# Kernel optimization log

Hardware: AMD Instinct MI355X
Metric: run time of the kernel (lower is better)

Reference implementation:

```python
import jax, jax.numpy as jnp
import numpy as np

NUM_CLASSES = 80
FOCAL_ALPHA = 0.25
FOCAL_GAMMA = 2.0
HUBER_SIGMA = 3.0
REG_MEAN = 0.0
REG_STD = 0.2
IMG_H = 800.0
IMG_W = 800.0
B, A, M = 4, 100000, 32


def setup_inputs() -> dict:
    key = jax.random.key(0)
    k1, k2, k3, k4, k5, k6, k7 = jax.random.split(key, 7)
    classification = jax.random.uniform(k1, (B, A, NUM_CLASSES), dtype=jnp.float32)
    regression = jax.random.normal(k2, (B, A, 4), dtype=jnp.float32)
    # plausible anchors: centers inside image, sizes 16..256
    cx = jax.random.uniform(k3, (A,), minval=0.0, maxval=IMG_W)
    cy = jax.random.uniform(k4, (A,), minval=0.0, maxval=IMG_H)
    s = jax.random.uniform(k5, (A, 2), minval=16.0, maxval=256.0)
    anchors = jnp.stack([cx - s[:, 0] / 2, cy - s[:, 1] / 2,
                         cx + s[:, 0] / 2, cy + s[:, 1] / 2], axis=1).astype(jnp.float32)
    # annotations: [B, M, 5] = x1,y1,x2,y2,class
    xy = jax.random.uniform(k6, (B, M, 2), minval=0.0, maxval=650.0)
    wh = jax.random.uniform(k7, (B, M, 2), minval=30.0, maxval=150.0)
    cls = jax.random.randint(jax.random.fold_in(key, 9), (B, M, 1), 0, NUM_CLASSES).astype(jnp.float32)
    annotations = jnp.concatenate([xy, xy + wh, cls], axis=-1)
    return {"classification": classification, "regression": regression,
            "anchors": anchors, "annotations": annotations}


def _pairwise_iou(anchors, boxes):
    # anchors [A,4], boxes [M,4] -> [A,M]
    ix1 = jnp.maximum(anchors[:, None, 0], boxes[None, :, 0])
    iy1 = jnp.maximum(anchors[:, None, 1], boxes[None, :, 1])
    ix2 = jnp.minimum(anchors[:, None, 2], boxes[None, :, 2])
    iy2 = jnp.minimum(anchors[:, None, 3], boxes[None, :, 3])
    inter = jnp.clip(ix2 - ix1, 0.0) * jnp.clip(iy2 - iy1, 0.0)
    area_a = (anchors[:, 2] - anchors[:, 0]) * (anchors[:, 3] - anchors[:, 1])
    area_b = (boxes[:, 2] - boxes[:, 0]) * (boxes[:, 3] - boxes[:, 1])
    union = area_a[:, None] + area_b[None, :] - inter
    return inter / jnp.maximum(union, 1e-8)


def _targets(anchors, annotations):
    # per-image anchor assignment, vmapped over batch
    def per_image(ann):
        boxes = ann[:, :4]
        cls = ann[:, 4].astype(jnp.int32)
        ious = _pairwise_iou(anchors, boxes)          # [A,M]
        best = jnp.argmax(ious, axis=1)               # [A]
        best_iou = jnp.max(ious, axis=1)
        pos = best_iou >= 0.5
        ign = (best_iou > 0.4) & (~pos)
        states = jnp.where(pos, 1.0, jnp.where(ign, -1.0, 0.0))
        cx = (anchors[:, 0] + anchors[:, 2]) * 0.5
        cy = (anchors[:, 1] + anchors[:, 3]) * 0.5
        inside = (cx >= 0) & (cx < IMG_W) & (cy >= 0) & (cy < IMG_H)
        states = jnp.where(inside, states, -1.0)
        labels = jax.nn.one_hot(cls[best], NUM_CLASSES, dtype=jnp.float32) * pos[:, None]
        ab = boxes[best]                              # assigned gt boxes [A,4]
        aw = anchors[:, 2] - anchors[:, 0]
        ah = anchors[:, 3] - anchors[:, 1]
        t = jnp.stack([(ab[:, 0] - anchors[:, 0]) / aw,
                       (ab[:, 1] - anchors[:, 1]) / ah,
                       (ab[:, 2] - anchors[:, 2]) / aw,
                       (ab[:, 3] - anchors[:, 3]) / ah], axis=1)
        t = (t - REG_MEAN) / REG_STD
        return labels, t, states
    return jax.vmap(per_image)(annotations)


def reference(classification, regression, anchors, annotations):
    labels, reg_t, states = _targets(anchors, annotations)   # [B,A,K],[B,A,4],[B,A]
    num_pos = jnp.maximum(jnp.sum((states == 1.0).astype(jnp.float32)), 1.0)
    # focal loss over non-ignored anchors
    valid = (states != -1.0)[..., None].astype(jnp.float32)
    p = jnp.clip(classification, 1e-4, 1.0 - 1e-4)
    bce = -(labels * jnp.log(p) + (1.0 - labels) * jnp.log1p(-p))
    alpha_f = jnp.where(labels == 1.0, FOCAL_ALPHA, 1.0 - FOCAL_ALPHA)
    focal_w = alpha_f * jnp.where(labels == 1.0, 1.0 - p, p) ** FOCAL_GAMMA
    cls_loss = jnp.sum(focal_w * bce * valid) / num_pos
    # smooth L1 over positive anchors
    pos_m = (states == 1.0)[..., None].astype(jnp.float32)
    s2 = HUBER_SIGMA ** 2
    d = jnp.abs(regression - reg_t)
    l1 = jnp.where(d < 1.0 / s2, 0.5 * s2 * d * d, d - 0.5 / s2)
    reg_loss = jnp.sum(l1 * pos_m) / num_pos
    return cls_loss + reg_loss
```

## Files before the change

### kernel.cpp

```cpp
#include <hip/hip_runtime.h>

#define BB 4
#define AA 100000
#define MM 32
#define NC 80
#define GX 391
#define NBLK (GX * BB)


__global__ __launch_bounds__(256) void fused_kernel(
    const float* __restrict__ anchors,
    const float* __restrict__ annotations,
    const float* __restrict__ regression,
    const float* __restrict__ cls,
    float* __restrict__ cls_part,
    float* __restrict__ reg_part,
    unsigned* __restrict__ pos_part)
{
    __shared__ float ann[MM * 5];
    __shared__ int scode[256];
    const int b = blockIdx.y;
    const int tid = threadIdx.x;
    if (tid < MM * 5) ann[tid] = annotations[b * MM * 5 + tid];
    __syncthreads();

    const int abase = blockIdx.x * 256;
    const int a = abase + tid;
    float reg_sum = 0.0f;
    int pos_cnt = 0;
    int code = -2;

    if (a < AA) {
        const float4 an = ((const float4*)anchors)[a];
        const float ax1 = an.x, ay1 = an.y, ax2 = an.z, ay2 = an.w;
        const float area_a = __fmul_rn(__fsub_rn(ax2, ax1), __fsub_rn(ay2, ay1));

        float best_iou = -1.0f;
        int best = 0;
        #pragma unroll
        for (int j = 0; j < MM; ++j) {
            const float bx1 = ann[j * 5 + 0];
            const float by1 = ann[j * 5 + 1];
            const float bx2 = ann[j * 5 + 2];
            const float by2 = ann[j * 5 + 3];
            const float ix1 = fmaxf(ax1, bx1);
            const float iy1 = fmaxf(ay1, by1);
            const float ix2 = fminf(ax2, bx2);
            const float iy2 = fminf(ay2, by2);
            const float iw = fmaxf(__fsub_rn(ix2, ix1), 0.0f);
            const float ih = fmaxf(__fsub_rn(iy2, iy1), 0.0f);
            const float inter = __fmul_rn(iw, ih);
            const float area_b = __fmul_rn(__fsub_rn(bx2, bx1), __fsub_rn(by2, by1));
            const float uni = __fsub_rn(__fadd_rn(area_a, area_b), inter);
            const float iou = __fdiv_rn(inter, fmaxf(uni, 1e-8f));
            if (iou > best_iou) { best_iou = iou; best = j; }
        }

        const bool pos = best_iou >= 0.5f;
        const bool ign = (best_iou > 0.4f) && !pos;
        const float cx = (ax1 + ax2) * 0.5f;
        const float cy = (ay1 + ay2) * 0.5f;
        const bool inside = (cx >= 0.0f) && (cx < 800.0f) && (cy >= 0.0f) && (cy < 800.0f);

        const bool valid = inside && !ign;
        if (valid) code = pos ? (int)ann[best * 5 + 4] : -1;

        if (pos && inside) {
            pos_cnt = 1;
            const float aw = ax2 - ax1;
            const float ah = ay2 - ay1;
            const float bx1 = ann[best * 5 + 0];
            const float by1 = ann[best * 5 + 1];
            const float bx2 = ann[best * 5 + 2];
            const float by2 = ann[best * 5 + 3];
            float t[4];
            t[0] = ((bx1 - ax1) / aw) / 0.2f;
            t[1] = ((by1 - ay1) / ah) / 0.2f;
            t[2] = ((bx2 - ax2) / aw) / 0.2f;
            t[3] = ((by2 - ay2) / ah) / 0.2f;
            const float* rg = regression + (((size_t)b * AA + a) * 4);
            #pragma unroll
            for (int k = 0; k < 4; ++k) {
                const float d = fabsf(rg[k] - t[k]);
                reg_sum += (d < (1.0f / 9.0f)) ? (4.5f * d * d) : (d - (0.5f / 9.0f));
            }
        }
    }
    scode[tid] = code;
    __syncthreads();

    float csum = 0.0f;
    const float4* base4 = (const float4*)cls + ((size_t)b * AA + abase) * 20;
    const int maxflat = (abase + 256 <= AA) ? (5120 - 1) : ((AA - abase) * 20 - 1);

    #pragma unroll
    for (int batch = 0; batch < 4; ++batch) {
        float4 v[5];
        #pragma unroll
        for (int k = 0; k < 5; ++k) {
            const int flat = (batch * 5 + k) * 256 + tid;
            v[k] = base4[min(flat, maxflat)];
        }
        #pragma unroll
        for (int k = 0; k < 5; ++k) {
            const int flat = (batch * 5 + k) * 256 + tid;
            const int s = flat / 20;
            const int colb = (flat - s * 20) * 4;
            const int c = scode[s];
            const float m = (c != -2) ? 1.0f : 0.0f;
            const float px[4] = { v[k].x, v[k].y, v[k].z, v[k].w };
            float pc[4];
            float sub = 0.0f;
            #pragma unroll
            for (int j = 0; j < 4; ++j) {
                const float p = fminf(fmaxf(px[j], 1e-4f), 0.9999f);
                pc[j] = p;
                sub += 0.75f * p * p * (-__logf(1.0f - p));
            }
            csum += m * sub;
            const unsigned rel = (unsigned)(c - colb);
            if (rel < 4u) {
                const float p = pc[rel];
                const float onem = 1.0f - p;
                csum += 0.25f * onem * onem * (-__logf(p))
                      - 0.75f * p * p * (-__logf(onem));
            }
        }
    }

    #pragma unroll
    for (int off = 32; off > 0; off >>= 1) {
        csum    += __shfl_down(csum, off);
        reg_sum += __shfl_down(reg_sum, off);
        pos_cnt += __shfl_down(pos_cnt, off);
    }
    __shared__ float wc[4], wr[4];
    __shared__ int   wp[4];
    const int wave = tid >> 6, lane = tid & 63;
    if (lane == 0) { wc[wave] = csum; wr[wave] = reg_sum; wp[wave] = pos_cnt; }
    __syncthreads();
    if (tid == 0) {
        const int idx = b * GX + blockIdx.x;
        cls_part[idx] = wc[0] + wc[1] + wc[2] + wc[3];
        reg_part[idx] = wr[0] + wr[1] + wr[2] + wr[3];
        pos_part[idx] = (unsigned)(wp[0] + wp[1] + wp[2] + wp[3]);
    }
}

__global__ __launch_bounds__(256) void finalize_kernel(
    const float* __restrict__ cls_part,
    const float* __restrict__ reg_part,
    const unsigned* __restrict__ pos_part,
    float* __restrict__ out)
{
    float cs = 0.0f, rs = 0.0f;
    unsigned pc = 0;
    for (int i = threadIdx.x; i < NBLK; i += 256) {
        cs += cls_part[i];
        rs += reg_part[i];
        pc += pos_part[i];
    }
    #pragma unroll
    for (int off = 32; off > 0; off >>= 1) {
        cs += __shfl_down(cs, off);
        rs += __shfl_down(rs, off);
        pc += __shfl_down(pc, off);
    }
    __shared__ float wc[4], wr[4];
    __shared__ unsigned wp[4];
    const int wave = threadIdx.x >> 6, lane = threadIdx.x & 63;
    if (lane == 0) { wc[wave] = cs; wr[wave] = rs; wp[wave] = pc; }
    __syncthreads();
    if (threadIdx.x == 0) {
        const float csum = wc[0] + wc[1] + wc[2] + wc[3];
        const float rsum = wr[0] + wr[1] + wr[2] + wr[3];
        const float np = fmaxf((float)(wp[0] + wp[1] + wp[2] + wp[3]), 1.0f);
        out[0] = (csum + rsum) / np;
    }
}

extern "C" void kernel_launch(void* const* d_in, const int* in_sizes, int n_in,
                              void* d_out, int out_size, void* d_ws, size_t ws_size,
                              hipStream_t stream)
{
    const float* classification = (const float*)d_in[0];
    const float* regression     = (const float*)d_in[1];
    const float* anchors        = (const float*)d_in[2];
    const float* annotations    = (const float*)d_in[3];
    float* out = (float*)d_out;

    float*    cls_part = (float*)d_ws;
    float*    reg_part = cls_part + NBLK;
    unsigned* pos_part = (unsigned*)(reg_part + NBLK);

    dim3 grid(GX, BB);
    fused_kernel<<<grid, 256, 0, stream>>>(anchors, annotations, regression,
                                           classification, cls_part, reg_part, pos_part);
    finalize_kernel<<<1, 256, 0, stream>>>(cls_part, reg_part, pos_part, out);
}
```

Measured before the change: 202.9 us.

## Split anchor assignment from focal loss and stream classification with strided flat loads

The fused kernel is split in two. A codes kernel computes per-anchor assignment codes into a byte array in workspace, along with the regression and positive-count partials. A separate focal kernel then streams the whole classification tensor with grid-strided float4 loads, reading each anchor's code from global memory instead of shared memory. It also switches to hardware log2 with a single ln2 scale at the end and folds the alpha constants into two accumulators. This adds an extra launch and a round trip for the code bytes, but decouples the IoU compute from the bandwidth-bound pass and gives more independent loads in flight.

```diff
diff --git a/kernel.cpp b/kernel.cpp
--- a/kernel.cpp
+++ b/kernel.cpp
@@ -6,29 +6,41 @@
 #define NC 80
 #define GX 391
 #define NBLK (GX * BB)
-
-
-__global__ __launch_bounds__(256) void fused_kernel(
+#define FB 3125
+#define FT (FB * 256)
+#define N4 (BB * AA * (NC/4))
+#define LN2 0.69314718055994530942f
+
+
+__device__ __forceinline__ float hw_log2(float x) {
+#if defined(__has_builtin)
+#if __has_builtin(__builtin_amdgcn_logf)
+    return __builtin_amdgcn_logf(x);
+#else
+    return __log2f(x);
+#endif
+#else
+    return __log2f(x);
+#endif
+}
+
+__global__ __launch_bounds__(256) void codes_kernel(
     const float* __restrict__ anchors,
     const float* __restrict__ annotations,
     const float* __restrict__ regression,
-    const float* __restrict__ cls,
-    float* __restrict__ cls_part,
     float* __restrict__ reg_part,
-    unsigned* __restrict__ pos_part)
+    unsigned* __restrict__ pos_part,
+    signed char* __restrict__ codes)
 {
     __shared__ float ann[MM * 5];
-    __shared__ int scode[256];
     const int b = blockIdx.y;
     const int tid = threadIdx.x;
     if (tid < MM * 5) ann[tid] = annotations[b * MM * 5 + tid];
     __syncthreads();
 
-    const int abase = blockIdx.x * 256;
-    const int a = abase + tid;
+    const int a = blockIdx.x * 256 + tid;
     float reg_sum = 0.0f;
     int pos_cnt = 0;
-    int code = -2;
 
     if (a < AA) {
         const float4 an = ((const float4*)anchors)[a];
@@ -62,8 +74,9 @@
         const float cy = (ay1 + ay2) * 0.5f;
         const bool inside = (cx >= 0.0f) && (cx < 800.0f) && (cy >= 0.0f) && (cy < 800.0f);
 
-        const bool valid = inside && !ign;
-        if (valid) code = pos ? (int)ann[best * 5 + 4] : -1;
+        int code = -2;
+        if (inside && !ign) code = pos ? (int)ann[best * 5 + 4] : -1;
+        codes[b * AA + a] = (signed char)code;
 
         if (pos && inside) {
             pos_cnt = 1;
@@ -86,80 +99,97 @@
             }
         }
     }
-    scode[tid] = code;
-    __syncthreads();
-
-    float csum = 0.0f;
-    const float4* base4 = (const float4*)cls + ((size_t)b * AA + abase) * 20;
-    const int maxflat = (abase + 256 <= AA) ? (5120 - 1) : ((AA - abase) * 20 - 1);
-
-    #pragma unroll
-    for (int batch = 0; batch < 4; ++batch) {
+
+    #pragma unroll
+    for (int off = 32; off > 0; off >>= 1) {
+        reg_sum += __shfl_down(reg_sum, off);
+        pos_cnt += __shfl_down(pos_cnt, off);
+    }
+    __shared__ float wr[4];
+    __shared__ int   wp[4];
+    const int wave = tid >> 6, lane = tid & 63;
+    if (lane == 0) { wr[wave] = reg_sum; wp[wave] = pos_cnt; }
+    __syncthreads();
+    if (tid == 0) {
+        const int idx = b * GX + blockIdx.x;
+        reg_part[idx] = wr[0] + wr[1] + wr[2] + wr[3];
+        pos_part[idx] = (unsigned)(wp[0] + wp[1] + wp[2] + wp[3]);
+    }
+}
+
+__global__ __launch_bounds__(256) void focal_kernel(
+    const float4* __restrict__ cls4,
+    const signed char* __restrict__ codes,
+    float* __restrict__ cls_part)
+{
+    const int t0 = blockIdx.x * 256 + threadIdx.x;
+    float csum2 = 0.0f;
+    float pcor2 = 0.0f;
+
+    #pragma unroll
+    for (int half = 0; half < 2; ++half) {
         float4 v[5];
+        int    cd[5];
         #pragma unroll
         for (int k = 0; k < 5; ++k) {
-            const int flat = (batch * 5 + k) * 256 + tid;
-            v[k] = base4[min(flat, maxflat)];
-        }
+            const int i = t0 + (half * 5 + k) * FT;
+            v[k]  = cls4[i];
+            cd[k] = codes[i / 20];
+        }
+        __builtin_amdgcn_sched_barrier(0);
         #pragma unroll
         for (int k = 0; k < 5; ++k) {
-            const int flat = (batch * 5 + k) * 256 + tid;
-            const int s = flat / 20;
-            const int colb = (flat - s * 20) * 4;
-            const int c = scode[s];
-            const float m = (c != -2) ? 1.0f : 0.0f;
-            const float px[4] = { v[k].x, v[k].y, v[k].z, v[k].w };
-            float pc[4];
-            float sub = 0.0f;
-            #pragma unroll
-            for (int j = 0; j < 4; ++j) {
-                const float p = fminf(fmaxf(px[j], 1e-4f), 0.9999f);
-                pc[j] = p;
-                sub += 0.75f * p * p * (-__logf(1.0f - p));
-            }
-            csum += m * sub;
+            const int i = t0 + (half * 5 + k) * FT;
+            const int s = i / 20;
+            const int colb = (i - s * 20) * 4;
+            const int c = cd[k];
+
+            const float p0 = fminf(fmaxf(v[k].x, 1e-4f), 0.9999f);
+            const float p1 = fminf(fmaxf(v[k].y, 1e-4f), 0.9999f);
+            const float p2 = fminf(fmaxf(v[k].z, 1e-4f), 0.9999f);
+            const float p3 = fminf(fmaxf(v[k].w, 1e-4f), 0.9999f);
+            const float l0 = hw_log2(1.0f - p0);
+            const float l1 = hw_log2(1.0f - p1);
+            const float l2 = hw_log2(1.0f - p2);
+            const float l3 = hw_log2(1.0f - p3);
+            float sub = -(p0 * p0 * l0);
+            sub -= p1 * p1 * l1;
+            sub -= p2 * p2 * l2;
+            sub -= p3 * p3 * l3;
+            csum2 += (c != -2) ? sub : 0.0f;
+
             const unsigned rel = (unsigned)(c - colb);
             if (rel < 4u) {
-                const float p = pc[rel];
+                const float p  = (rel & 2u) ? ((rel & 1u) ? p3 : p2) : ((rel & 1u) ? p1 : p0);
+                const float ln = (rel & 2u) ? ((rel & 1u) ? l3 : l2) : ((rel & 1u) ? l1 : l0);
                 const float onem = 1.0f - p;
-                csum += 0.25f * onem * onem * (-__logf(p))
-                      - 0.75f * p * p * (-__logf(onem));
+                pcor2 -= onem * onem * hw_log2(p);
+                csum2 += p * p * ln;
             }
         }
     }
 
-    #pragma unroll
-    for (int off = 32; off > 0; off >>= 1) {
-        csum    += __shfl_down(csum, off);
-        reg_sum += __shfl_down(reg_sum, off);
-        pos_cnt += __shfl_down(pos_cnt, off);
-    }
-    __shared__ float wc[4], wr[4];
-    __shared__ int   wp[4];
-    const int wave = tid >> 6, lane = tid & 63;
-    if (lane == 0) { wc[wave] = csum; wr[wave] = reg_sum; wp[wave] = pos_cnt; }
-    __syncthreads();
-    if (tid == 0) {
-        const int idx = b * GX + blockIdx.x;
-        cls_part[idx] = wc[0] + wc[1] + wc[2] + wc[3];
-        reg_part[idx] = wr[0] + wr[1] + wr[2] + wr[3];
-        pos_part[idx] = (unsigned)(wp[0] + wp[1] + wp[2] + wp[3]);
-    }
+    float csum = LN2 * (0.75f * csum2 + 0.25f * pcor2);
+
+    #pragma unroll
+    for (int off = 32; off > 0; off >>= 1) csum += __shfl_down(csum, off);
+    __shared__ float wc[4];
+    const int wave = threadIdx.x >> 6, lane = threadIdx.x & 63;
+    if (lane == 0) wc[wave] = csum;
+    __syncthreads();
+    if (threadIdx.x == 0) cls_part[blockIdx.x] = wc[0] + wc[1] + wc[2] + wc[3];
 }
 
 __global__ __launch_bounds__(256) void finalize_kernel(
-    const float* __restrict__ cls_part,
     const float* __restrict__ reg_part,
     const unsigned* __restrict__ pos_part,
+    const float* __restrict__ cls_part,
     float* __restrict__ out)
 {
     float cs = 0.0f, rs = 0.0f;
     unsigned pc = 0;
-    for (int i = threadIdx.x; i < NBLK; i += 256) {
-        cs += cls_part[i];
-        rs += reg_part[i];
-        pc += pos_part[i];
-    }
+    for (int i = threadIdx.x; i < FB; i += 256) cs += cls_part[i];
+    for (int i = threadIdx.x; i < NBLK; i += 256) { rs += reg_part[i]; pc += pos_part[i]; }
     #pragma unroll
     for (int off = 32; off > 0; off >>= 1) {
         cs += __shfl_down(cs, off);
@@ -189,12 +219,14 @@
     const float* annotations    = (const float*)d_in[3];
     float* out = (float*)d_out;
 
-    float*    cls_part = (float*)d_ws;
-    float*    reg_part = cls_part + NBLK;
-    unsigned* pos_part = (unsigned*)(reg_part + NBLK);
-
-    dim3 grid(GX, BB);
-    fused_kernel<<<grid, 256, 0, stream>>>(anchors, annotations, regression,
-                                           classification, cls_part, reg_part, pos_part);
-    finalize_kernel<<<1, 256, 0, stream>>>(cls_part, reg_part, pos_part, out);
-}
+    float*       reg_part = (float*)d_ws;
+    unsigned*    pos_part = (unsigned*)d_ws + NBLK;
+    float*       cls_part = (float*)d_ws + 2 * NBLK;
+    signed char* codes    = (signed char*)d_ws + 65536;
+
+    dim3 gA(GX, BB);
+    codes_kernel<<<gA, 256, 0, stream>>>(anchors, annotations, regression,
+                                         reg_part, pos_part, codes);
+    focal_kernel<<<FB, 256, 0, stream>>>((const float4*)classification, codes, cls_part);
+    finalize_kernel<<<1, 256, 0, stream>>>(reg_part, pos_part, cls_part, out);
+}
```

Measured after the change: 210.2 us. 1.04x slower.
